# Performance work log

Hardware: AMD Instinct MI355X
Metric: run time of the kernel (lower is better)

## Reference

```python
import jax, jax.numpy as jnp
import numpy as np

B, D, H = 4096, 1024, 1024
LN_EPS = 1e-5


def setup_inputs() -> dict:
    key = jax.random.key(0)
    ks = jax.random.split(key, 5)
    return {
        "x": jax.random.normal(ks[0], (B, D), dtype=jnp.float32),
        "prev_h": jax.random.normal(ks[1], (B, H), dtype=jnp.float32),
        "prev_c": jax.random.normal(ks[2], (B, H), dtype=jnp.float32),
        "Wx": jax.random.normal(ks[3], (D, 4 * H), dtype=jnp.float32) * 0.01,
        "Wh": jax.random.normal(ks[4], (H, 4 * H), dtype=jnp.float32) * 0.01,
        "b": jnp.zeros((4 * H,), dtype=jnp.float32),
        "ln_gamma": jnp.ones((4 * H,), dtype=jnp.float32),
        "ln_beta": jnp.zeros((4 * H,), dtype=jnp.float32),
    }


def reference(x, prev_h, prev_c, Wx, Wh, b, ln_gamma, ln_beta):
    # pre-activations: [B, 4H]
    a = x @ Wx + prev_h @ Wh + b
    # LayerNorm over last dim (use_ln=True)
    mu = jnp.mean(a, axis=-1, keepdims=True)
    var = jnp.mean(jnp.square(a - mu), axis=-1, keepdims=True)
    a = (a - mu) * jax.lax.rsqrt(var + LN_EPS) * ln_gamma + ln_beta
    i = jax.nn.sigmoid(a[:, :H])
    f = jax.nn.sigmoid(a[:, H:2 * H])
    o = jax.nn.sigmoid(a[:, 2 * H:3 * H])
    g = jnp.tanh(a[:, 3 * H:])
    next_c = f * prev_c + i * g
    next_h = o * jnp.tanh(next_c)
    # dropout=0.0 -> identity
    return (next_h, next_c)
```

## Files before the change

### kernel.cpp

```cpp
#include <hip/hip_runtime.h>
#include <hip/hip_bf16.h>
#include <stdint.h>

typedef unsigned short u16;
typedef __attribute__((ext_vector_type(8))) short short8;
typedef __attribute__((ext_vector_type(4))) float f32x4;

#define B_DIM 4096
#define D_DIM 1024
#define H_DIM 1024
#define K_DIM 2048
#define N_DIM 4096
#define LN_EPS 1e-5f

__device__ __forceinline__ u16 f2bf(float f) {
    union { float f; uint32_t u; } v; v.f = f;
    uint32_t u = v.u;
    uint32_t r = (u + 0x7FFFu + ((u >> 16) & 1u)) >> 16;
    return (u16)r;
}
__device__ __forceinline__ float bf2f(u16 h) {
    union { uint32_t u; float f; } v; v.u = ((uint32_t)h) << 16;
    return v.f;
}
__device__ __forceinline__ void gld16(const u16* g, u16* l) {
    __builtin_amdgcn_global_load_lds(
        (const __attribute__((address_space(1))) void*)g,
        (__attribute__((address_space(3))) void*)l,
        16, 0, 0);
}
__device__ __forceinline__ float sigm(float x) { return 1.0f / (1.0f + __expf(-x)); }
__device__ __forceinline__ float tanh_fast(float x) { return 1.0f - 2.0f / (__expf(2.0f * x) + 1.0f); }

__global__ __launch_bounds__(256) void cast_concat_A(const float* __restrict__ x,
                                                     const float* __restrict__ h,
                                                     u16* __restrict__ A) {
    int id = blockIdx.x * 256 + threadIdx.x;
    int row = id >> 8;
    int col = (id & 255) * 8;
    const float* src = (col < D_DIM) ? (x + (size_t)row * D_DIM + col)
                                     : (h + (size_t)row * H_DIM + (col - D_DIM));
    float4 v0 = ((const float4*)src)[0];
    float4 v1 = ((const float4*)src)[1];
    union { u16 us[8]; uint4 u; } p;
    p.us[0] = f2bf(v0.x); p.us[1] = f2bf(v0.y); p.us[2] = f2bf(v0.z); p.us[3] = f2bf(v0.w);
    p.us[4] = f2bf(v1.x); p.us[5] = f2bf(v1.y); p.us[6] = f2bf(v1.z); p.us[7] = f2bf(v1.w);
    *(uint4*)(A + (size_t)id * 8) = p.u;
}

__global__ __launch_bounds__(256) void cast_transpose_B(const float* __restrict__ Wx,
                                                        const float* __restrict__ Wh,
                                                        u16* __restrict__ Bt) {
    __shared__ u16 tile[64 * 64];
    const int n0 = blockIdx.x * 64;
    const int k0 = blockIdx.y * 64;
    const int t = threadIdx.x;
    const int kl  = t >> 4;
    const int nl4 = (t & 15) * 4;
#pragma unroll
    for (int it = 0; it < 4; ++it) {
        const int klocal = kl + it * 16;
        const int k = k0 + klocal;
        const float* src = (k < D_DIM) ? (Wx + (size_t)k * N_DIM)
                                       : (Wh + (size_t)(k - D_DIM) * N_DIM);
        float4 v = *(const float4*)(src + n0 + nl4);
        union { u16 us[4]; uint2 u; } p;
        p.us[0] = f2bf(v.x); p.us[1] = f2bf(v.y); p.us[2] = f2bf(v.z); p.us[3] = f2bf(v.w);
        const int swz = 8 * ((klocal >> 4) & 3);
        *(uint2*)(tile + klocal * 64 + (nl4 ^ swz)) = p.u;
    }
    __syncthreads();
    const int nl = t >> 2;
    const int kp = (t & 3) * 16;
    const int swz = 8 * (t & 3);
    union { u16 us[16]; uint4 q[2]; } o;
#pragma unroll
    for (int i = 0; i < 16; ++i)
        o.us[i] = tile[(kp + i) * 64 + (nl ^ swz)];
    u16* dst = Bt + (size_t)(n0 + nl) * K_DIM + k0 + kp;
    *(uint4*)dst = o.q[0];
    *(uint4*)(dst + 8) = o.q[1];
}

__global__ __launch_bounds__(256) void gemm_bf16(const u16* __restrict__ A,
                                                 const u16* __restrict__ Bt,
                                                 const float* __restrict__ bias,
                                                 u16* __restrict__ C) {
    __shared__ u16 As[128 * 32];
    __shared__ u16 Bs[128 * 32];
    const int m0 = blockIdx.y * 128;
    const int n0 = blockIdx.x * 128;
    const int tid = threadIdx.x;
    const int wave = tid >> 6, lane = tid & 63;
    const int wm = (wave & 1) * 64, wn = (wave >> 1) * 64;

    f32x4 acc[4][4] = {};

    const int srow = wave * 32 + (lane >> 2);
    const int skc  = (((lane & 3) - ((lane >> 3) & 3)) & 3) * 8;
    const u16* aG = A  + (size_t)(m0 + srow) * K_DIM + skc;
    const u16* bG = Bt + (size_t)(n0 + srow) * K_DIM + skc;
    u16* aL = As + (wave * 32) * 32;
    u16* bL = Bs + (wave * 32) * 32;

    const int lr  = lane & 15;
    const int krd = (((lane >> 4) + (lr >> 1)) & 3) * 8;

    for (int kt = 0; kt < K_DIM; kt += 32) {
        __syncthreads();
        gld16(aG + kt,                aL);
        gld16(aG + kt + 16 * K_DIM,   aL + 16 * 32);
        gld16(bG + kt,                bL);
        gld16(bG + kt + 16 * K_DIM,   bL + 16 * 32);
        __syncthreads();

        short8 af[4], bfr[4];
#pragma unroll
        for (int i = 0; i < 4; ++i)
            af[i] = *(const short8*)(As + (wm + i * 16 + lr) * 32 + krd);
#pragma unroll
        for (int j = 0; j < 4; ++j)
            bfr[j] = *(const short8*)(Bs + (wn + j * 16 + lr) * 32 + krd);
#pragma unroll
        for (int i = 0; i < 4; ++i)
#pragma unroll
            for (int j = 0; j < 4; ++j)
                acc[i][j] = __builtin_amdgcn_mfma_f32_16x16x32_bf16(af[i], bfr[j], acc[i][j], 0, 0, 0);
    }

#pragma unroll
    for (int i = 0; i < 4; ++i) {
        const int r0 = m0 + wm + i * 16 + (lane >> 4) * 4;
#pragma unroll
        for (int j = 0; j < 4; ++j) {
            const int c = n0 + wn + j * 16 + (lane & 15);
            const float bb = bias[c];
#pragma unroll
            for (int r = 0; r < 4; ++r)
                C[(size_t)(r0 + r) * N_DIM + c] = f2bf(acc[i][j][r] + bb);
        }
    }
}

__global__ __launch_bounds__(256) void ln_lstm(const u16* __restrict__ aT,
                                               const float* __restrict__ pc,
                                               const float* __restrict__ gamma,
                                               const float* __restrict__ beta,
                                               float* __restrict__ out) {
    const int row = blockIdx.x;
    const int t = threadIdx.x;
    const u16* ar = aT + (size_t)row * N_DIM;
    const int j0 = t * 4;

    union U2 { uint2 u; u16 us[4]; };
    U2 g4[4];
#pragma unroll
    for (int s = 0; s < 4; ++s) g4[s].u = *(const uint2*)(ar + s * H_DIM + j0);

    float sum = 0.f, ssq = 0.f;
#pragma unroll
    for (int s = 0; s < 4; ++s)
#pragma unroll
        for (int e = 0; e < 4; ++e) { float v = bf2f(g4[s].us[e]); sum += v; ssq += v * v; }

#pragma unroll
    for (int off = 32; off > 0; off >>= 1) {
        sum += __shfl_down(sum, off, 64);
        ssq += __shfl_down(ssq, off, 64);
    }
    __shared__ float red[8];
    if ((t & 63) == 0) { red[t >> 6] = sum; red[4 + (t >> 6)] = ssq; }
    __syncthreads();
    const float ts = red[0] + red[1] + red[2] + red[3];
    const float tq = red[4] + red[5] + red[6] + red[7];
    const float mu = ts * (1.0f / N_DIM);
    const float var = fmaxf(tq * (1.0f / N_DIM) - mu * mu, 0.0f);
    const float rs = rsqrtf(var + LN_EPS);

    float vi[4], vf[4], vo[4], vg[4];
    auto gate = [&](int s, float* v) {
        const int off = s * H_DIM;
        float4 gm = *(const float4*)(gamma + off + j0);
        float4 bt = *(const float4*)(beta + off + j0);
        v[0] = (bf2f(g4[s].us[0]) - mu) * rs * gm.x + bt.x;
        v[1] = (bf2f(g4[s].us[1]) - mu) * rs * gm.y + bt.y;
        v[2] = (bf2f(g4[s].us[2]) - mu) * rs * gm.z + bt.z;
        v[3] = (bf2f(g4[s].us[3]) - mu) * rs * gm.w + bt.w;
    };
    gate(0, vi); gate(1, vf); gate(2, vo); gate(3, vg);

    float4 c4 = *(const float4*)(pc + (size_t)row * H_DIM + j0);
    float cin[4] = {c4.x, c4.y, c4.z, c4.w};
    float nh[4], nc[4];
#pragma unroll
    for (int r = 0; r < 4; ++r) {
        float ig = sigm(vi[r]);
        float fg = sigm(vf[r]);
        float og = sigm(vo[r]);
        float gg = tanh_fast(vg[r]);
        nc[r] = fg * cin[r] + ig * gg;
        nh[r] = og * tanh_fast(nc[r]);
    }
    float4 h4 = {nh[0], nh[1], nh[2], nh[3]};
    float4 c4o = {nc[0], nc[1], nc[2], nc[3]};
    *(float4*)(out + (size_t)row * H_DIM + j0) = h4;
    *(float4*)(out + (size_t)B_DIM * H_DIM + (size_t)row * H_DIM + j0) = c4o;
}

extern "C" void kernel_launch(void* const* d_in, const int* in_sizes, int n_in,
                              void* d_out, int out_size, void* d_ws, size_t ws_size,
                              hipStream_t stream) {
    const float* x  = (const float*)d_in[0];
    const float* ph = (const float*)d_in[1];
    const float* pc = (const float*)d_in[2];
    const float* Wx = (const float*)d_in[3];
    const float* Wh = (const float*)d_in[4];
    const float* b  = (const float*)d_in[5];
    const float* gm = (const float*)d_in[6];
    const float* bt = (const float*)d_in[7];
    float* out = (float*)d_out;

    char* ws = (char*)d_ws;
    u16* Abf = (u16*)ws;
    u16* Btb = (u16*)(ws + (size_t)16 * 1024 * 1024);
    u16* aT  = (u16*)(ws + (size_t)32 * 1024 * 1024);

    cast_concat_A<<<dim3(4096), dim3(256), 0, stream>>>(x, ph, Abf);
    cast_transpose_B<<<dim3(64, 32), dim3(256), 0, stream>>>(Wx, Wh, Btb);
    gemm_bf16<<<dim3(32, 32), dim3(256), 0, stream>>>(Abf, Btb, b, aT);
    ln_lstm<<<dim3(4096), dim3(256), 0, stream>>>(aT, pc, gm, bt, out);
}
```

Baseline: 235.2 us.

## Use 32x32x16 MFMA with 64-wide K tiles and merge prep kernels

The two fp32-to-bf16 prep kernels (activation concat and weight transpose) are merged into one launch that branches on block index, saving a kernel launch. The GEMM now stages K tiles of 64 instead of 32 with a new XOR-style swizzle, halving the number of barrier pairs per K sweep. It also switches from 16x16x32 to 32x32x16 MFMA with 2x2 accumulators of 16 floats each, which cuts LDS fragment reads per MFMA. The costs are double the LDS footprint and a reworked epilogue index mapping that must match the 32x32 accumulator layout.

```diff
diff --git a/kernel.cpp b/kernel.cpp
--- a/kernel.cpp
+++ b/kernel.cpp
@@ -4,7 +4,7 @@
 
 typedef unsigned short u16;
 typedef __attribute__((ext_vector_type(8))) short short8;
-typedef __attribute__((ext_vector_type(4))) float f32x4;
+typedef __attribute__((ext_vector_type(16))) float f32x16;
 
 #define B_DIM 4096
 #define D_DIM 1024
@@ -32,112 +32,122 @@
 __device__ __forceinline__ float sigm(float x) { return 1.0f / (1.0f + __expf(-x)); }
 __device__ __forceinline__ float tanh_fast(float x) { return 1.0f - 2.0f / (__expf(2.0f * x) + 1.0f); }
 
-__global__ __launch_bounds__(256) void cast_concat_A(const float* __restrict__ x,
-                                                     const float* __restrict__ h,
-                                                     u16* __restrict__ A) {
-    int id = blockIdx.x * 256 + threadIdx.x;
-    int row = id >> 8;
-    int col = (id & 255) * 8;
-    const float* src = (col < D_DIM) ? (x + (size_t)row * D_DIM + col)
-                                     : (h + (size_t)row * H_DIM + (col - D_DIM));
-    float4 v0 = ((const float4*)src)[0];
-    float4 v1 = ((const float4*)src)[1];
-    union { u16 us[8]; uint4 u; } p;
-    p.us[0] = f2bf(v0.x); p.us[1] = f2bf(v0.y); p.us[2] = f2bf(v0.z); p.us[3] = f2bf(v0.w);
-    p.us[4] = f2bf(v1.x); p.us[5] = f2bf(v1.y); p.us[6] = f2bf(v1.z); p.us[7] = f2bf(v1.w);
-    *(uint4*)(A + (size_t)id * 8) = p.u;
-}
-
-__global__ __launch_bounds__(256) void cast_transpose_B(const float* __restrict__ Wx,
-                                                        const float* __restrict__ Wh,
-                                                        u16* __restrict__ Bt) {
+__global__ __launch_bounds__(256) void prep(const float* __restrict__ x,
+                                            const float* __restrict__ h,
+                                            const float* __restrict__ Wx,
+                                            const float* __restrict__ Wh,
+                                            u16* __restrict__ A,
+                                            u16* __restrict__ Bt) {
     __shared__ u16 tile[64 * 64];
-    const int n0 = blockIdx.x * 64;
-    const int k0 = blockIdx.y * 64;
     const int t = threadIdx.x;
-    const int kl  = t >> 4;
-    const int nl4 = (t & 15) * 4;
-#pragma unroll
-    for (int it = 0; it < 4; ++it) {
-        const int klocal = kl + it * 16;
-        const int k = k0 + klocal;
-        const float* src = (k < D_DIM) ? (Wx + (size_t)k * N_DIM)
-                                       : (Wh + (size_t)(k - D_DIM) * N_DIM);
-        float4 v = *(const float4*)(src + n0 + nl4);
-        union { u16 us[4]; uint2 u; } p;
-        p.us[0] = f2bf(v.x); p.us[1] = f2bf(v.y); p.us[2] = f2bf(v.z); p.us[3] = f2bf(v.w);
-        const int swz = 8 * ((klocal >> 4) & 3);
-        *(uint2*)(tile + klocal * 64 + (nl4 ^ swz)) = p.u;
-    }
-    __syncthreads();
-    const int nl = t >> 2;
-    const int kp = (t & 3) * 16;
-    const int swz = 8 * (t & 3);
-    union { u16 us[16]; uint4 q[2]; } o;
-#pragma unroll
-    for (int i = 0; i < 16; ++i)
-        o.us[i] = tile[(kp + i) * 64 + (nl ^ swz)];
-    u16* dst = Bt + (size_t)(n0 + nl) * K_DIM + k0 + kp;
-    *(uint4*)dst = o.q[0];
-    *(uint4*)(dst + 8) = o.q[1];
+    if (blockIdx.x < 4096) {
+        int id = blockIdx.x * 256 + t;
+        int row = id >> 8;
+        int col = (id & 255) * 8;
+        const float* src = (col < D_DIM) ? (x + (size_t)row * D_DIM + col)
+                                         : (h + (size_t)row * H_DIM + (col - D_DIM));
+        float4 v0 = ((const float4*)src)[0];
+        float4 v1 = ((const float4*)src)[1];
+        union { u16 us[8]; uint4 u; } p;
+        p.us[0] = f2bf(v0.x); p.us[1] = f2bf(v0.y); p.us[2] = f2bf(v0.z); p.us[3] = f2bf(v0.w);
+        p.us[4] = f2bf(v1.x); p.us[5] = f2bf(v1.y); p.us[6] = f2bf(v1.z); p.us[7] = f2bf(v1.w);
+        *(uint4*)(A + (size_t)id * 8) = p.u;
+    } else {
+        const int v = blockIdx.x - 4096;
+        const int n0 = (v & 63) * 64;
+        const int k0 = (v >> 6) * 64;
+        const int kl  = t >> 4;
+        const int nl4 = (t & 15) * 4;
+#pragma unroll
+        for (int it = 0; it < 4; ++it) {
+            const int klocal = kl + it * 16;
+            const int k = k0 + klocal;
+            const float* src = (k < D_DIM) ? (Wx + (size_t)k * N_DIM)
+                                           : (Wh + (size_t)(k - D_DIM) * N_DIM);
+            float4 w = *(const float4*)(src + n0 + nl4);
+            union { u16 us[4]; uint2 u; } p;
+            p.us[0] = f2bf(w.x); p.us[1] = f2bf(w.y); p.us[2] = f2bf(w.z); p.us[3] = f2bf(w.w);
+            const int swz = 8 * ((klocal >> 4) & 3);
+            *(uint2*)(tile + klocal * 64 + (nl4 ^ swz)) = p.u;
+        }
+        __syncthreads();
+        const int nl = t >> 2;
+        const int kp = (t & 3) * 16;
+        const int swz = 8 * (t & 3);
+        union { u16 us[16]; uint4 q[2]; } o;
+#pragma unroll
+        for (int i = 0; i < 16; ++i)
+            o.us[i] = tile[(kp + i) * 64 + (nl ^ swz)];
+        u16* dst = Bt + (size_t)(n0 + nl) * K_DIM + k0 + kp;
+        *(uint4*)dst = o.q[0];
+        *(uint4*)(dst + 8) = o.q[1];
+    }
 }
 
 __global__ __launch_bounds__(256) void gemm_bf16(const u16* __restrict__ A,
                                                  const u16* __restrict__ Bt,
                                                  const float* __restrict__ bias,
                                                  u16* __restrict__ C) {
-    __shared__ u16 As[128 * 32];
-    __shared__ u16 Bs[128 * 32];
+    __shared__ u16 As[128 * 64];
+    __shared__ u16 Bs[128 * 64];
     const int m0 = blockIdx.y * 128;
     const int n0 = blockIdx.x * 128;
     const int tid = threadIdx.x;
     const int wave = tid >> 6, lane = tid & 63;
     const int wm = (wave & 1) * 64, wn = (wave >> 1) * 64;
 
-    f32x4 acc[4][4] = {};
-
-    const int srow = wave * 32 + (lane >> 2);
-    const int skc  = (((lane & 3) - ((lane >> 3) & 3)) & 3) * 8;
-    const u16* aG = A  + (size_t)(m0 + srow) * K_DIM + skc;
-    const u16* bG = Bt + (size_t)(n0 + srow) * K_DIM + skc;
-    u16* aL = As + (wave * 32) * 32;
-    u16* bL = Bs + (wave * 32) * 32;
-
-    const int lr  = lane & 15;
-    const int krd = (((lane >> 4) + (lr >> 1)) & 3) * 8;
-
-    for (int kt = 0; kt < K_DIM; kt += 32) {
+    f32x16 acc[2][2] = {};
+
+    const int kbg = ((lane & 7) - ((lane >> 3) & 7)) & 7;
+    const int skc = kbg * 8;
+    const u16* aG = A  + (size_t)(m0 + wave * 32 + (lane >> 3)) * K_DIM + skc;
+    const u16* bG = Bt + (size_t)(n0 + wave * 32 + (lane >> 3)) * K_DIM + skc;
+    u16* aL = As + (wave * 32) * 64;
+    u16* bL = Bs + (wave * 32) * 64;
+
+    const int lr = lane & 31;
+    const int half = lane >> 5;
+    const u16* aFbase = As + (size_t)(wm + lr) * 64;
+    const u16* bFbase = Bs + (size_t)(wn + lr) * 64;
+
+    for (int kt = 0; kt < K_DIM; kt += 64) {
         __syncthreads();
-        gld16(aG + kt,                aL);
-        gld16(aG + kt + 16 * K_DIM,   aL + 16 * 32);
-        gld16(bG + kt,                bL);
-        gld16(bG + kt + 16 * K_DIM,   bL + 16 * 32);
+#pragma unroll
+        for (int q = 0; q < 4; ++q) {
+            gld16(aG + kt + (size_t)q * 8 * K_DIM, aL + q * 8 * 64);
+            gld16(bG + kt + (size_t)q * 8 * K_DIM, bL + q * 8 * 64);
+        }
         __syncthreads();
 
-        short8 af[4], bfr[4];
-#pragma unroll
-        for (int i = 0; i < 4; ++i)
-            af[i] = *(const short8*)(As + (wm + i * 16 + lr) * 32 + krd);
-#pragma unroll
-        for (int j = 0; j < 4; ++j)
-            bfr[j] = *(const short8*)(Bs + (wn + j * 16 + lr) * 32 + krd);
-#pragma unroll
-        for (int i = 0; i < 4; ++i)
-#pragma unroll
-            for (int j = 0; j < 4; ++j)
-                acc[i][j] = __builtin_amdgcn_mfma_f32_16x16x32_bf16(af[i], bfr[j], acc[i][j], 0, 0, 0);
-    }
-
-#pragma unroll
-    for (int i = 0; i < 4; ++i) {
-        const int r0 = m0 + wm + i * 16 + (lane >> 4) * 4;
-#pragma unroll
-        for (int j = 0; j < 4; ++j) {
-            const int c = n0 + wn + j * 16 + (lane & 15);
+#pragma unroll
+        for (int kk = 0; kk < 4; ++kk) {
+            const int koff = (((kk * 2 + half) + (lr & 7)) & 7) * 8;
+            short8 af[2], bf[2];
+#pragma unroll
+            for (int i = 0; i < 2; ++i)
+                af[i] = *(const short8*)(aFbase + i * 32 * 64 + koff);
+#pragma unroll
+            for (int j = 0; j < 2; ++j)
+                bf[j] = *(const short8*)(bFbase + j * 32 * 64 + koff);
+#pragma unroll
+            for (int i = 0; i < 2; ++i)
+#pragma unroll
+                for (int j = 0; j < 2; ++j)
+                    acc[i][j] = __builtin_amdgcn_mfma_f32_32x32x16_bf16(af[i], bf[j], acc[i][j], 0, 0, 0);
+        }
+    }
+
+#pragma unroll
+    for (int i = 0; i < 2; ++i) {
+#pragma unroll
+        for (int j = 0; j < 2; ++j) {
+            const int c = n0 + wn + 32 * j + lr;
             const float bb = bias[c];
 #pragma unroll
-            for (int r = 0; r < 4; ++r)
-                C[(size_t)(r0 + r) * N_DIM + c] = f2bf(acc[i][j][r] + bb);
+            for (int reg = 0; reg < 16; ++reg) {
+                const int row = m0 + wm + 32 * i + (reg & 3) + 8 * (reg >> 2) + 4 * half;
+                C[(size_t)row * N_DIM + c] = f2bf(acc[i][j][reg] + bb);
+            }
         }
     }
 }
@@ -225,8 +235,7 @@
     u16* Btb = (u16*)(ws + (size_t)16 * 1024 * 1024);
     u16* aT  = (u16*)(ws + (size_t)32 * 1024 * 1024);
 
-    cast_concat_A<<<dim3(4096), dim3(256), 0, stream>>>(x, ph, Abf);
-    cast_transpose_B<<<dim3(64, 32), dim3(256), 0, stream>>>(Wx, Wh, Btb);
+    prep<<<dim3(4096 + 2048), dim3(256), 0, stream>>>(x, ph, Wx, Wh, Abf, Btb);
     gemm_bf16<<<dim3(32, 32), dim3(256), 0, stream>>>(Abf, Btb, b, aT);
     ln_lstm<<<dim3(4096), dim3(256), 0, stream>>>(aT, pc, gm, bt, out);
 }
```

New measurement: 229.5 us. 2.5% less time.

## Multi-stage LDS pipeline in GEMM and merge prep kernels into one launch

Applied to the files above, without the earlier changes.

The GEMM main loop now uses a four-slot LDS ring buffer. It prefetches global-to-LDS loads two K-steps ahead, with a partial vmcnt wait and a single barrier per iteration instead of two barriers around each synchronous load. The two cast kernels for A and B are merged into one launch with a block-index split. The change aims to hide global load latency behind MFMA work and cut one launch. In exchange it uses 64KB of LDS per block, which can limit occupancy, and it issues two redundant wraparound loads at the tail.

```diff
diff --git a/kernel.cpp b/kernel.cpp
--- a/kernel.cpp
+++ b/kernel.cpp
@@ -32,66 +32,68 @@
 __device__ __forceinline__ float sigm(float x) { return 1.0f / (1.0f + __expf(-x)); }
 __device__ __forceinline__ float tanh_fast(float x) { return 1.0f - 2.0f / (__expf(2.0f * x) + 1.0f); }
 
-__global__ __launch_bounds__(256) void cast_concat_A(const float* __restrict__ x,
-                                                     const float* __restrict__ h,
-                                                     u16* __restrict__ A) {
-    int id = blockIdx.x * 256 + threadIdx.x;
-    int row = id >> 8;
-    int col = (id & 255) * 8;
-    const float* src = (col < D_DIM) ? (x + (size_t)row * D_DIM + col)
-                                     : (h + (size_t)row * H_DIM + (col - D_DIM));
-    float4 v0 = ((const float4*)src)[0];
-    float4 v1 = ((const float4*)src)[1];
-    union { u16 us[8]; uint4 u; } p;
-    p.us[0] = f2bf(v0.x); p.us[1] = f2bf(v0.y); p.us[2] = f2bf(v0.z); p.us[3] = f2bf(v0.w);
-    p.us[4] = f2bf(v1.x); p.us[5] = f2bf(v1.y); p.us[6] = f2bf(v1.z); p.us[7] = f2bf(v1.w);
-    *(uint4*)(A + (size_t)id * 8) = p.u;
-}
-
-__global__ __launch_bounds__(256) void cast_transpose_B(const float* __restrict__ Wx,
-                                                        const float* __restrict__ Wh,
-                                                        u16* __restrict__ Bt) {
+__global__ __launch_bounds__(256) void prep(const float* __restrict__ x,
+                                            const float* __restrict__ h,
+                                            const float* __restrict__ Wx,
+                                            const float* __restrict__ Wh,
+                                            u16* __restrict__ A,
+                                            u16* __restrict__ Bt) {
     __shared__ u16 tile[64 * 64];
-    const int n0 = blockIdx.x * 64;
-    const int k0 = blockIdx.y * 64;
     const int t = threadIdx.x;
-    const int kl  = t >> 4;
-    const int nl4 = (t & 15) * 4;
-#pragma unroll
-    for (int it = 0; it < 4; ++it) {
-        const int klocal = kl + it * 16;
-        const int k = k0 + klocal;
-        const float* src = (k < D_DIM) ? (Wx + (size_t)k * N_DIM)
-                                       : (Wh + (size_t)(k - D_DIM) * N_DIM);
-        float4 v = *(const float4*)(src + n0 + nl4);
-        union { u16 us[4]; uint2 u; } p;
-        p.us[0] = f2bf(v.x); p.us[1] = f2bf(v.y); p.us[2] = f2bf(v.z); p.us[3] = f2bf(v.w);
-        const int swz = 8 * ((klocal >> 4) & 3);
-        *(uint2*)(tile + klocal * 64 + (nl4 ^ swz)) = p.u;
-    }
-    __syncthreads();
-    const int nl = t >> 2;
-    const int kp = (t & 3) * 16;
-    const int swz = 8 * (t & 3);
-    union { u16 us[16]; uint4 q[2]; } o;
-#pragma unroll
-    for (int i = 0; i < 16; ++i)
-        o.us[i] = tile[(kp + i) * 64 + (nl ^ swz)];
-    u16* dst = Bt + (size_t)(n0 + nl) * K_DIM + k0 + kp;
-    *(uint4*)dst = o.q[0];
-    *(uint4*)(dst + 8) = o.q[1];
+    if (blockIdx.x < 4096) {
+        int id = blockIdx.x * 256 + t;
+        int row = id >> 8;
+        int col = (id & 255) * 8;
+        const float* src = (col < D_DIM) ? (x + (size_t)row * D_DIM + col)
+                                         : (h + (size_t)row * H_DIM + (col - D_DIM));
+        float4 v0 = ((const float4*)src)[0];
+        float4 v1 = ((const float4*)src)[1];
+        union { u16 us[8]; uint4 u; } p;
+        p.us[0] = f2bf(v0.x); p.us[1] = f2bf(v0.y); p.us[2] = f2bf(v0.z); p.us[3] = f2bf(v0.w);
+        p.us[4] = f2bf(v1.x); p.us[5] = f2bf(v1.y); p.us[6] = f2bf(v1.z); p.us[7] = f2bf(v1.w);
+        *(uint4*)(A + (size_t)id * 8) = p.u;
+    } else {
+        const int v = blockIdx.x - 4096;
+        const int n0 = (v & 63) * 64;
+        const int k0 = (v >> 6) * 64;
+        const int kl  = t >> 4;
+        const int nl4 = (t & 15) * 4;
+#pragma unroll
+        for (int it = 0; it < 4; ++it) {
+            const int klocal = kl + it * 16;
+            const int k = k0 + klocal;
+            const float* src = (k < D_DIM) ? (Wx + (size_t)k * N_DIM)
+                                           : (Wh + (size_t)(k - D_DIM) * N_DIM);
+            float4 w = *(const float4*)(src + n0 + nl4);
+            union { u16 us[4]; uint2 u; } p;
+            p.us[0] = f2bf(w.x); p.us[1] = f2bf(w.y); p.us[2] = f2bf(w.z); p.us[3] = f2bf(w.w);
+            const int swz = 8 * ((klocal >> 4) & 3);
+            *(uint2*)(tile + klocal * 64 + (nl4 ^ swz)) = p.u;
+        }
+        __syncthreads();
+        const int nl = t >> 2;
+        const int kp = (t & 3) * 16;
+        const int swz = 8 * (t & 3);
+        union { u16 us[16]; uint4 q[2]; } o;
+#pragma unroll
+        for (int i = 0; i < 16; ++i)
+            o.us[i] = tile[(kp + i) * 64 + (nl ^ swz)];
+        u16* dst = Bt + (size_t)(n0 + nl) * K_DIM + k0 + kp;
+        *(uint4*)dst = o.q[0];
+        *(uint4*)(dst + 8) = o.q[1];
+    }
 }
 
 __global__ __launch_bounds__(256) void gemm_bf16(const u16* __restrict__ A,
                                                  const u16* __restrict__ Bt,
                                                  const float* __restrict__ bias,
                                                  u16* __restrict__ C) {
-    __shared__ u16 As[128 * 32];
-    __shared__ u16 Bs[128 * 32];
+    __shared__ u16 As[4][4096];
+    __shared__ u16 Bs[4][4096];
+    const int tid = threadIdx.x;
+    const int wave = tid >> 6, lane = tid & 63;
     const int m0 = blockIdx.y * 128;
     const int n0 = blockIdx.x * 128;
-    const int tid = threadIdx.x;
-    const int wave = tid >> 6, lane = tid & 63;
     const int wm = (wave & 1) * 64, wn = (wave >> 1) * 64;
 
     f32x4 acc[4][4] = {};
@@ -100,32 +102,42 @@
     const int skc  = (((lane & 3) - ((lane >> 3) & 3)) & 3) * 8;
     const u16* aG = A  + (size_t)(m0 + srow) * K_DIM + skc;
     const u16* bG = Bt + (size_t)(n0 + srow) * K_DIM + skc;
-    u16* aL = As + (wave * 32) * 32;
-    u16* bL = Bs + (wave * 32) * 32;
+    const int ldsoff = (wave * 32) * 32;
 
     const int lr  = lane & 15;
     const int krd = (((lane >> 4) + (lr >> 1)) & 3) * 8;
 
-    for (int kt = 0; kt < K_DIM; kt += 32) {
-        __syncthreads();
-        gld16(aG + kt,                aL);
-        gld16(aG + kt + 16 * K_DIM,   aL + 16 * 32);
-        gld16(bG + kt,                bL);
-        gld16(bG + kt + 16 * K_DIM,   bL + 16 * 32);
-        __syncthreads();
-
-        short8 af[4], bfr[4];
+    auto stage = [&](int t) {
+        const int kt = (t & 63) * 32;
+        u16* aL = &As[t & 3][ldsoff];
+        u16* bL = &Bs[t & 3][ldsoff];
+        gld16(aG + kt,               aL);
+        gld16(aG + kt + 16 * K_DIM,  aL + 16 * 32);
+        gld16(bG + kt,               bL);
+        gld16(bG + kt + 16 * K_DIM,  bL + 16 * 32);
+    };
+
+    stage(0);
+    stage(1);
+    for (int it = 0; it < 64; ++it) {
+        stage(it + 2);
+        __builtin_amdgcn_s_waitcnt(0xF78);
+        __builtin_amdgcn_s_barrier();
+        __builtin_amdgcn_sched_barrier(0);
+
+        const int s = it & 3;
+        short8 af[4], bf[4];
 #pragma unroll
         for (int i = 0; i < 4; ++i)
-            af[i] = *(const short8*)(As + (wm + i * 16 + lr) * 32 + krd);
+            af[i] = *(const short8*)(&As[s][(wm + i * 16 + lr) * 32 + krd]);
 #pragma unroll
         for (int j = 0; j < 4; ++j)
-            bfr[j] = *(const short8*)(Bs + (wn + j * 16 + lr) * 32 + krd);
+            bf[j] = *(const short8*)(&Bs[s][(wn + j * 16 + lr) * 32 + krd]);
 #pragma unroll
         for (int i = 0; i < 4; ++i)
 #pragma unroll
             for (int j = 0; j < 4; ++j)
-                acc[i][j] = __builtin_amdgcn_mfma_f32_16x16x32_bf16(af[i], bfr[j], acc[i][j], 0, 0, 0);
+                acc[i][j] = __builtin_amdgcn_mfma_f32_16x16x32_bf16(af[i], bf[j], acc[i][j], 0, 0, 0);
     }
 
 #pragma unroll
@@ -133,7 +145,7 @@
         const int r0 = m0 + wm + i * 16 + (lane >> 4) * 4;
 #pragma unroll
         for (int j = 0; j < 4; ++j) {
-            const int c = n0 + wn + j * 16 + (lane & 15);
+            const int c = n0 + wn + j * 16 + lr;
             const float bb = bias[c];
 #pragma unroll
             for (int r = 0; r < 4; ++r)
@@ -225,8 +237,7 @@
     u16* Btb = (u16*)(ws + (size_t)16 * 1024 * 1024);
     u16* aT  = (u16*)(ws + (size_t)32 * 1024 * 1024);
 
-    cast_concat_A<<<dim3(4096), dim3(256), 0, stream>>>(x, ph, Abf);
-    cast_transpose_B<<<dim3(64, 32), dim3(256), 0, stream>>>(Wx, Wh, Btb);
+    prep<<<dim3(4096 + 2048), dim3(256), 0, stream>>>(x, ph, Wx, Wh, Abf, Btb);
     gemm_bf16<<<dim3(32, 32), dim3(256), 0, stream>>>(Abf, Btb, b, aT);
     ln_lstm<<<dim3(4096), dim3(256), 0, stream>>>(aT, pc, gm, bt, out);
 }
```

Result: slower. 240.2 us (+2.1%).
